# Kernel optimization log

Measured on AMD Instinct MI355X. Metric: run time of the kernel, lower is better.

## Reference

```python
import jax, jax.numpy as jnp
import numpy as np

# PGA G(3,0,1) blade layout: [1, e0,e1,e2,e3, e01,e02,e03,e12,e13,e23, e012,e013,e023,e123, e0123]
GRADE = jnp.array([0, 1, 1, 1, 1, 2, 2, 2, 2, 2, 2, 3, 3, 3, 3, 4])
# invariant inner product uses only blades not containing the degenerate e0
INNER_IDX = jnp.array([0, 2, 3, 4, 8, 9, 10, 14])

B, N, IN_MV, IN_S = 1, 1024, 16, 128
H, HID_MV, HID_S = 8, 4, 32
C_Z, OUT_MV, OUT_S = 128, 16, 128
ROPE_BASE = 4096.0


def equi_linear(mv, w5):
    # grade-wise equivariant channel mixing: w5 [out, in, 5] -> per-blade weight [out, in, 16]
    w16 = w5[:, :, GRADE]
    return jnp.einsum('...ib,oib->...ob', mv, w16)


def rope(x, base=ROPE_BASE):
    # rotary positional encoding along item axis 1; last dim must be even
    n, d = x.shape[1], x.shape[-1]
    half = d // 2
    freqs = base ** (-jnp.arange(half, dtype=x.dtype) / half)
    ang = jnp.arange(n, dtype=x.dtype)[:, None] * freqs  # [N, half]
    shp = (1, n) + (1,) * (x.ndim - 3) + (half,)
    cos, sin = jnp.cos(ang).reshape(shp), jnp.sin(ang).reshape(shp)
    x1, x2 = x[..., 0::2], x[..., 1::2]
    return jnp.stack([x1 * cos - x2 * sin, x1 * sin + x2 * cos], axis=-1).reshape(x.shape)


def setup_inputs() -> dict:
    key = jax.random.key(0)
    ks = jax.random.split(key, 16)
    sc_mv = 1.0 / np.sqrt(IN_MV)
    sc_s = 1.0 / np.sqrt(IN_S)
    return {
        'mv': jax.random.normal(ks[0], (B, N, IN_MV, 16), jnp.float32),
        's': jax.random.normal(ks[1], (B, N, IN_S), jnp.float32),
        'z': jax.random.normal(ks[2], (B, N, N, C_Z), jnp.float32),
        'q_w_mv': jax.random.normal(ks[3], (H * HID_MV, IN_MV, 5), jnp.float32) * sc_mv,
        'q_w_s': jax.random.normal(ks[4], (H * HID_S, IN_S), jnp.float32) * sc_s,
        'k_w_mv': jax.random.normal(ks[5], (HID_MV, IN_MV, 5), jnp.float32) * sc_mv,
        'k_w_s': jax.random.normal(ks[6], (HID_S, IN_S), jnp.float32) * sc_s,
        'v_w_mv': jax.random.normal(ks[7], (HID_MV, IN_MV, 5), jnp.float32) * sc_mv,
        'v_w_s': jax.random.normal(ks[8], (HID_S, IN_S), jnp.float32) * sc_s,
        'out_w_mv': jax.random.normal(ks[9], (OUT_MV, H * HID_MV, 5), jnp.float32) / np.sqrt(H * HID_MV),
        'out_w_s': jax.random.normal(ks[10], (OUT_S, H * HID_S), jnp.float32) / np.sqrt(H * HID_S),
        'ln_g': jnp.ones((C_Z,), jnp.float32),
        'ln_b': jnp.zeros((C_Z,), jnp.float32),
        'bias_w': jax.random.normal(ks[11], (C_Z, H), jnp.float32) / np.sqrt(C_Z),
    }


def reference(mv, s, z, q_w_mv, q_w_s, k_w_mv, k_w_s, v_w_mv, v_w_s,
              out_w_mv, out_w_s, ln_g, ln_b, bias_w):
    b, n = mv.shape[0], mv.shape[1]
    # multi-query QKV: queries per-head, shared single-head K/V
    q_mv = equi_linear(mv, q_w_mv).reshape(b, n, H, HID_MV, 16)
    q_s = jnp.einsum('bns,os->bno', s, q_w_s).reshape(b, n, H, HID_S)
    k_mv = equi_linear(mv, k_w_mv)                     # [B,N,hid_mv,16]
    k_s = jnp.einsum('bns,os->bno', s, k_w_s)          # [B,N,hid_s]
    v_mv = equi_linear(mv, v_w_mv)
    v_s = jnp.einsum('bns,os->bno', s, v_w_s)
    # rotary encoding on scalar queries/keys
    q_s, k_s = rope(q_s), rope(k_s)
    # invariant attention features: non-degenerate mv components + scalars
    qf = jnp.concatenate([q_mv[..., INNER_IDX].reshape(b, n, H, HID_MV * 8), q_s], axis=-1)
    kf = jnp.concatenate([k_mv[..., INNER_IDX].reshape(b, n, HID_MV * 8), k_s], axis=-1)
    d = qf.shape[-1]
    logits = jnp.einsum('bqhd,bkd->bhqk', qf, kf) / jnp.sqrt(jnp.asarray(d, qf.dtype))
    # pair bias: Linear(LayerNorm(z)) -> heads
    mu = jnp.mean(z, axis=-1, keepdims=True)
    var = jnp.var(z, axis=-1, keepdims=True)
    zn = (z - mu) * jax.lax.rsqrt(var + 1e-5) * ln_g + ln_b
    bias = jnp.einsum('bqkc,ch->bhqk', zn, bias_w)
    attn = jax.nn.softmax(logits + bias, axis=-1)      # [B,H,N,N]
    o_mv = jnp.einsum('bhqk,bkcx->bqhcx', attn, v_mv).reshape(b, n, H * HID_MV, 16)
    o_s = jnp.einsum('bhqk,bkc->bqhc', attn, v_s).reshape(b, n, H * HID_S)
    out_mv = equi_linear(o_mv, out_w_mv)               # [B,N,out_mv,16]
    out_s = jnp.einsum('bnc,oc->bno', o_s, out_w_s)    # [B,N,out_s]
    return out_mv, out_s
```

## Files before the change

### kernel.cpp

```cpp
#include <hip/hip_runtime.h>
#include <hip/hip_bf16.h>

__device__ __constant__ int GRADE_C[16] = {0,1,1,1,1,2,2,2,2,2,2,3,3,3,3,4};
__device__ __constant__ int INNER_C[8]  = {0,2,3,4,8,9,10,14};

#define OFF_GH    0
#define GWBT_BYTE 4096
#define KFB_BYTE  16384
#define VTB_BYTE  262144
#define QFB_BYTE  524288

typedef __attribute__((ext_vector_type(8))) short bf16x8;
typedef __attribute__((ext_vector_type(4))) float f32x4;
typedef __attribute__((ext_vector_type(4))) unsigned int u32x4;

static __device__ __forceinline__ unsigned short f2bf(float f) {
    unsigned int u = __float_as_uint(f);
    u = u + 0x7fffu + ((u >> 16) & 1u);
    return (unsigned short)(u >> 16);
}
static __device__ __forceinline__ unsigned pk2(float lo, float hi) {
    return (unsigned)f2bf(lo) | ((unsigned)f2bf(hi) << 16);
}
static __device__ __forceinline__ unsigned cvtpk(float lo, float hi) {
    __hip_bfloat162 c = __float22bfloat162_rn(make_float2(lo, hi));
    unsigned u;
    __builtin_memcpy(&u, &c, 4);
    return u;
}
static __device__ __forceinline__ float bflo(unsigned int u) {
    return __uint_as_float(u << 16);
}
static __device__ __forceinline__ float bfhi(unsigned int u) {
    return __uint_as_float(u & 0xffff0000u);
}

#define LDS_BAR() do { \
    asm volatile("s_waitcnt lgkmcnt(0)" ::: "memory"); \
    __builtin_amdgcn_s_barrier(); \
} while (0)

__global__ __launch_bounds__(256) void kproj(
    const float* __restrict__ mv, const float* __restrict__ s,
    const float* __restrict__ q_w_mv, const float* __restrict__ q_w_s,
    const float* __restrict__ k_w_mv, const float* __restrict__ k_w_s,
    const float* __restrict__ v_w_mv, const float* __restrict__ v_w_s,
    const float* __restrict__ ln_g, const float* __restrict__ ln_b,
    const float* __restrict__ bias_w, float* __restrict__ ws)
{
    __shared__ __align__(16) float mvn[256];
    __shared__ __align__(16) float sn[128];
    __shared__ float qs_pre[256];
    __shared__ float ks_pre[32];
    __shared__ float vs_pre[32];
    const int n = blockIdx.x, t = threadIdx.x;

    unsigned short* kfb = (unsigned short*)((char*)ws + KFB_BYTE);
    unsigned short* qfb = (unsigned short*)((char*)ws + QFB_BYTE);
    unsigned short* gwp = (unsigned short*)((char*)ws + GWBT_BYTE);
    unsigned short* vtb = (unsigned short*)((char*)ws + VTB_BYTE);

    mvn[t] = mv[n * 256 + t];
    if (t < 128) sn[t] = s[n * 128 + t];
    __syncthreads();

    {
        const float4* w = (const float4*)(q_w_s + t * 128);
        const float4* sv = (const float4*)sn;
        float acc = 0.f;
        #pragma unroll
        for (int c4 = 0; c4 < 32; ++c4) {
            float4 wv = w[c4], x = sv[c4];
            acc += wv.x * x.x + wv.y * x.y + wv.z * x.z + wv.w * x.w;
        }
        qs_pre[t] = acc;
    }
    if (t < 64) {
        const float* wb = (t < 32) ? (k_w_s + t * 128) : (v_w_s + (t - 32) * 128);
        const float4* w = (const float4*)wb;
        const float4* sv = (const float4*)sn;
        float acc = 0.f;
        #pragma unroll
        for (int c4 = 0; c4 < 32; ++c4) {
            float4 wv = w[c4], x = sv[c4];
            acc += wv.x * x.x + wv.y * x.y + wv.z * x.z + wv.w * x.w;
        }
        if (t < 32) ks_pre[t] = acc; else vs_pre[t - 32] = acc;
    }
    {
        int o = t >> 3, j = t & 7;
        int bx = INNER_C[j], g = GRADE_C[bx];
        float acc = 0.f;
        #pragma unroll
        for (int i = 0; i < 16; ++i)
            acc += mvn[i * 16 + bx] * q_w_mv[(o * 16 + i) * 5 + g];
        int h = o >> 2, c = o & 3, d = c * 8 + j;
        qfb[n * 1024 + h * 64 + d] = f2bf(acc);
    }
    {
        int hp = 8 + (t >> 5), d = t & 31;
        qfb[n * 1024 + hp * 64 + d] = 0;
        qfb[n * 1024 + hp * 64 + 32 + d] = 0;
    }
    if (t < 32) {
        int bx = INNER_C[t & 7], g = GRADE_C[bx];
        float acc = 0.f;
        #pragma unroll
        for (int i = 0; i < 16; ++i)
            acc += mvn[i * 16 + bx] * k_w_mv[((t >> 3) * 16 + i) * 5 + g];
        kfb[n * 64 + t] = f2bf(acc);
    }
    if (t >= 64 && t < 128) {
        int idx = t - 64, x = idx & 15, g = GRADE_C[x];
        float acc = 0.f;
        #pragma unroll
        for (int i = 0; i < 16; ++i)
            acc += mvn[i * 16 + x] * v_w_mv[((idx >> 4) * 16 + i) * 5 + g];
        vtb[idx * 1024 + n] = f2bf(acc);
    }
    __syncthreads();

    {
        int h = t >> 5, dd = t & 31, i = dd >> 1;
        float freq = exp2f(-0.75f * (float)i);
        float ang = (float)n * freq;
        float cv = cosf(ang), sv = sinf(ang);
        float x1 = qs_pre[h * 32 + 2 * i], x2 = qs_pre[h * 32 + 2 * i + 1];
        float val = ((dd & 1) == 0) ? (x1 * cv - x2 * sv) : (x1 * sv + x2 * cv);
        qfb[n * 1024 + h * 64 + 32 + dd] = f2bf(val);
    }
    if (t < 32) {
        int i = t >> 1;
        float freq = exp2f(-0.75f * (float)i);
        float ang = (float)n * freq;
        float cv = cosf(ang), sv = sinf(ang);
        float x1 = ks_pre[2 * i], x2 = ks_pre[2 * i + 1];
        float val = ((t & 1) == 0) ? (x1 * cv - x2 * sv) : (x1 * sv + x2 * cv);
        kfb[n * 64 + 32 + t] = f2bf(val);
    }
    if (t >= 32 && t < 64) vtb[(64 + t - 32) * 1024 + n] = f2bf(vs_pre[t - 32]);

    if (n == 0) {
        if (t < 128) {
            int cb = t >> 5, r = t & 31;
            int lg, e;
            if (r < 16) { lg = r >> 2; e = r & 3; }
            else        { lg = (r - 16) >> 2; e = 4 + (r & 3); }
            int pos = cb * 32 + lg * 8 + e;
            float g = ln_g[t];
            #pragma unroll
            for (int j = 0; j < 8; ++j)
                gwp[j * 128 + pos] = f2bf(g * bias_w[t * 8 + j]);
            gwp[8 * 128 + pos] = 0x3F80;
            #pragma unroll
            for (int j = 9; j < 16; ++j) gwp[j * 128 + pos] = 0;
        }
        if (t >= 128 && t < 136) {
            int h = t - 128;
            float gh = 0.f, ch = 0.f;
            for (int c = 0; c < 128; ++c) {
                gh += ln_g[c] * bias_w[c * 8 + h];
                ch += ln_b[c] * bias_w[c * 8 + h];
            }
            ws[OFF_GH + h] = gh;
            ws[OFF_GH + 8 + h] = ch;
        }
    }
}

__global__ __launch_bounds__(256, 3) void kfused(
    const float* __restrict__ z, const float* __restrict__ ws,
    const float* __restrict__ out_w_mv, const float* __restrict__ out_w_s,
    float* __restrict__ d_out)
{
    __shared__ float d1[128][17];
    __shared__ float d2[128][17];
    __shared__ float ssq[128];
    __shared__ float GhCh_s[16];
    __shared__ __align__(16) unsigned int Pb[8 * 512];
    __shared__ float inv_l[8];
    __shared__ float o_sh[8 * 96];

    const int q = blockIdx.x, t = threadIdx.x;
    const int w = t >> 6, l = t & 63, lm = l & 15, lg = l >> 4;

    if (t < 16) GhCh_s[t] = ws[OFF_GH + t];

    bf16x8 B1[4], B2[2];
    #pragma unroll
    for (int ks = 0; ks < 4; ++ks)
        B1[ks] = *(const bf16x8*)((const char*)ws + GWBT_BYTE + (lm * 128 + ks * 32 + lg * 8) * 2);
    #pragma unroll
    for (int ds = 0; ds < 2; ++ds)
        B2[ds] = *(const bf16x8*)((const char*)ws + QFB_BYTE + ((size_t)q * 1024 + lm * 64 + ds * 32 + lg * 8) * 2);

    const unsigned short* kfb = (const unsigned short*)((const char*)ws + KFB_BYTE);

    for (int kb = 0; kb < 8; ++kb) {
        float4 za[2][4], zb[2][4];
        bf16x8 A2[2][2];
        #pragma unroll
        for (int mi = 0; mi < 2; ++mi) {
            const int krow = kb * 128 + (w * 2 + mi) * 16 + lm;
            const float* zr = z + ((size_t)q * 1024 + krow) * 128 + lg * 4;
            #pragma unroll
            for (int ks = 0; ks < 4; ++ks) {
                za[mi][ks] = *(const float4*)(zr + ks * 32);
                zb[mi][ks] = *(const float4*)(zr + ks * 32 + 16);
            }
            #pragma unroll
            for (int ds = 0; ds < 2; ++ds)
                A2[mi][ds] = *(const bf16x8*)(kfb + (size_t)krow * 64 + ds * 32 + lg * 8);
        }

        if (kb > 0 && t < 128) {
            const int p = t >> 1, hg = t & 1;
            const int rr0 = 2 * p, rr1 = rr0 + 1;
            float mean0 = d1[rr0][8] * (1.f / 128.f);
            float var0  = ssq[rr0] * (1.f / 128.f) - mean0 * mean0;
            float rs0   = rsqrtf(var0 + 1e-5f);
            float mean1 = d1[rr1][8] * (1.f / 128.f);
            float var1  = ssq[rr1] * (1.f / 128.f) - mean1 * mean1;
            float rs1   = rsqrtf(var1 + 1e-5f);
            const int wbase = (kb - 1) * 64 + p;
            #pragma unroll
            for (int j = 0; j < 4; ++j) {
                int h = hg * 4 + j;
                float b0 = rs0 * (d1[rr0][h] - mean0 * GhCh_s[h]) + GhCh_s[8 + h];
                float s0 = d2[rr0][h] * 0.125f + b0;
                float b1 = rs1 * (d1[rr1][h] - mean1 * GhCh_s[h]) + GhCh_s[8 + h];
                float s1 = d2[rr1][h] * 0.125f + b1;
                Pb[h * 512 + (wbase ^ (h << 2))] = pk2(s0, s1);
            }
        }
        LDS_BAR();

        #pragma unroll
        for (int mi = 0; mi < 2; ++mi) {
            const int mt = w * 2 + mi;
            f32x4 acc1 = {0.f, 0.f, 0.f, 0.f};
            f32x4 acc2 = {0.f, 0.f, 0.f, 0.f};
            float sq = 0.f;
            #pragma unroll
            for (int ks = 0; ks < 4; ++ks) {
                float4 A = za[mi][ks], Bv = zb[mi][ks];
                sq = __builtin_fmaf(A.x, A.x, sq);   sq = __builtin_fmaf(A.y, A.y, sq);
                sq = __builtin_fmaf(A.z, A.z, sq);   sq = __builtin_fmaf(A.w, A.w, sq);
                sq = __builtin_fmaf(Bv.x, Bv.x, sq); sq = __builtin_fmaf(Bv.y, Bv.y, sq);
                sq = __builtin_fmaf(Bv.z, Bv.z, sq); sq = __builtin_fmaf(Bv.w, Bv.w, sq);
                u32x4 au;
                au[0] = cvtpk(A.x, A.y);   au[1] = cvtpk(A.z, A.w);
                au[2] = cvtpk(Bv.x, Bv.y); au[3] = cvtpk(Bv.z, Bv.w);
                bf16x8 af = __builtin_bit_cast(bf16x8, au);
                acc1 = __builtin_amdgcn_mfma_f32_16x16x32_bf16(af, B1[ks], acc1, 0, 0, 0);
            }
            acc2 = __builtin_amdgcn_mfma_f32_16x16x32_bf16(A2[mi][0], B2[0], acc2, 0, 0, 0);
            acc2 = __builtin_amdgcn_mfma_f32_16x16x32_bf16(A2[mi][1], B2[1], acc2, 0, 0, 0);

            sq += __shfl_xor(sq, 16);
            sq += __shfl_xor(sq, 32);
            if (lg == 0) ssq[mt * 16 + lm] = sq;

            #pragma unroll
            for (int r = 0; r < 4; ++r) {
                int row = mt * 16 + lg * 4 + r;
                d1[row][lm] = acc1[r];
                d2[row][lm] = acc2[r];
            }
        }
        LDS_BAR();
    }

    if (t < 128) {
        const int p = t >> 1, hg = t & 1;
        const int rr0 = 2 * p, rr1 = rr0 + 1;
        float mean0 = d1[rr0][8] * (1.f / 128.f);
        float var0  = ssq[rr0] * (1.f / 128.f) - mean0 * mean0;
        float rs0   = rsqrtf(var0 + 1e-5f);
        float mean1 = d1[rr1][8] * (1.f / 128.f);
        float var1  = ssq[rr1] * (1.f / 128.f) - mean1 * mean1;
        float rs1   = rsqrtf(var1 + 1e-5f);
        const int wbase = 7 * 64 + p;
        #pragma unroll
        for (int j = 0; j < 4; ++j) {
            int h = hg * 4 + j;
            float b0 = rs0 * (d1[rr0][h] - mean0 * GhCh_s[h]) + GhCh_s[8 + h];
            float s0 = d2[rr0][h] * 0.125f + b0;
            float b1 = rs1 * (d1[rr1][h] - mean1 * GhCh_s[h]) + GhCh_s[8 + h];
            float s1 = d2[rr1][h] * 0.125f + b1;
            Pb[h * 512 + (wbase ^ (h << 2))] = pk2(s0, s1);
        }
    }
    __syncthreads();

    {
        const int h = t >> 5, e = t & 31, hx = h << 2;
        unsigned int* Ph = &Pb[h * 512];
        float m = -1e30f;
        #pragma unroll
        for (int j = 0; j < 16; ++j) {
            unsigned int v = Ph[(e + j * 32) ^ hx];
            m = fmaxf(m, fmaxf(bflo(v), bfhi(v)));
        }
        #pragma unroll
        for (int d = 16; d >= 1; d >>= 1) m = fmaxf(m, __shfl_xor(m, d));
        float lsum = 0.f;
        #pragma unroll
        for (int j = 0; j < 16; ++j) {
            int idx = (e + j * 32) ^ hx;
            unsigned int v = Ph[idx];
            float p0 = __expf(bflo(v) - m);
            float p1 = __expf(bfhi(v) - m);
            lsum += p0 + p1;
            Ph[idx] = pk2(p0, p1);
        }
        #pragma unroll
        for (int d = 16; d >= 1; d >>= 1) lsum += __shfl_xor(lsum, d);
        if (e == 0) inv_l[h] = 1.f / lsum;
    }
    __syncthreads();

    {
        const unsigned short* vtb = (const unsigned short*)((const char*)ws + VTB_BYTE);
        const char* PbB = (const char*)Pb;
        const int hh = lm & 7;
        const int nmt = (w < 2) ? 2 : 1;
        for (int ii = 0; ii < nmt; ++ii) {
            int mt = w + ii * 4;
            f32x4 acc = {0.f, 0.f, 0.f, 0.f};
            #pragma unroll 8
            for (int ks = 0; ks < 32; ++ks) {
                bf16x8 a = *(const bf16x8*)(vtb + (size_t)(mt * 16 + lm) * 1024 + ks * 32 + lg * 8);
                bf16x8 b = *(const bf16x8*)(PbB + hh * 2048 + ((ks * 64 + lg * 16) ^ (hh << 4)));
                acc = __builtin_amdgcn_mfma_f32_16x16x32_bf16(a, b, acc, 0, 0, 0);
            }
            if (lm < 8) {
                float il = inv_l[lm];
                #pragma unroll
                for (int r = 0; r < 4; ++r)
                    o_sh[lm * 96 + mt * 16 + lg * 4 + r] = acc[r] * il;
            }
        }
    }
    __syncthreads();

    {
        int o2 = t >> 4, b = t & 15, g = GRADE_C[b];
        float acc = 0.f;
        #pragma unroll
        for (int i = 0; i < 32; ++i)
            acc += o_sh[(i >> 2) * 96 + (i & 3) * 16 + b] *
                   out_w_mv[(o2 * 32 + i) * 5 + g];
        d_out[(q * 16 + o2) * 16 + b] = acc;
    }
    if (t < 128) {
        const float* wv2 = out_w_s + t * 256;
        float acc = 0.f;
        #pragma unroll 4
        for (int c = 0; c < 256; ++c)
            acc += o_sh[(c >> 5) * 96 + 64 + (c & 31)] * wv2[c];
        d_out[262144 + q * 128 + t] = acc;
    }
}

extern "C" void kernel_launch(void* const* d_in, const int* in_sizes, int n_in,
                              void* d_out, int out_size, void* d_ws, size_t ws_size,
                              hipStream_t stream) {
    (void)in_sizes; (void)n_in; (void)out_size; (void)ws_size;
    const float* mv       = (const float*)d_in[0];
    const float* s        = (const float*)d_in[1];
    const float* z        = (const float*)d_in[2];
    const float* q_w_mv   = (const float*)d_in[3];
    const float* q_w_s    = (const float*)d_in[4];
    const float* k_w_mv   = (const float*)d_in[5];
    const float* k_w_s    = (const float*)d_in[6];
    const float* v_w_mv   = (const float*)d_in[7];
    const float* v_w_s    = (const float*)d_in[8];
    const float* out_w_mv = (const float*)d_in[9];
    const float* out_w_s  = (const float*)d_in[10];
    const float* ln_g     = (const float*)d_in[11];
    const float* ln_b     = (const float*)d_in[12];
    const float* bias_w   = (const float*)d_in[13];
    float* ws  = (float*)d_ws;
    float* out = (float*)d_out;

    kproj<<<1024, 256, 0, stream>>>(mv, s, q_w_mv, q_w_s, k_w_mv, k_w_s,
                                    v_w_mv, v_w_s, ln_g, ln_b, bias_w, ws);
    kfused<<<1024, 256, 0, stream>>>(z, ws, out_w_mv, out_w_s, out);
}
```

Baseline: 178.1 us.

## Register double-buffer z loads and finalize pair bias in-wave with shuffles

Replaces the 8-iteration loop, which staged MFMA results through LDS (d1/d2/ssq) with two block barriers per iteration, with 16 phases of 64 rows each. Each wave computes LayerNorm statistics and the bias/logit combination directly from its MFMA accumulators using lane shuffles, then writes packed bf16 scores to Pb. The next phase's z tile is prefetched into a second register buffer while the current one is processed. This removes the per-iteration barriers and LDS round trips so that loading z overlaps with compute, at the cost of more vector registers, which may lower occupancy under launch_bounds(256,3).

```diff
diff --git a/kernel.cpp b/kernel.cpp
--- a/kernel.cpp
+++ b/kernel.cpp
@@ -34,11 +34,6 @@
 static __device__ __forceinline__ float bfhi(unsigned int u) {
     return __uint_as_float(u & 0xffff0000u);
 }
-
-#define LDS_BAR() do { \
-    asm volatile("s_waitcnt lgkmcnt(0)" ::: "memory"); \
-    __builtin_amdgcn_s_barrier(); \
-} while (0)
 
 __global__ __launch_bounds__(256) void kproj(
     const float* __restrict__ mv, const float* __restrict__ s,
@@ -173,18 +168,12 @@
     const float* __restrict__ out_w_mv, const float* __restrict__ out_w_s,
     float* __restrict__ d_out)
 {
-    __shared__ float d1[128][17];
-    __shared__ float d2[128][17];
-    __shared__ float ssq[128];
-    __shared__ float GhCh_s[16];
     __shared__ __align__(16) unsigned int Pb[8 * 512];
     __shared__ float inv_l[8];
     __shared__ float o_sh[8 * 96];
 
     const int q = blockIdx.x, t = threadIdx.x;
     const int w = t >> 6, l = t & 63, lm = l & 15, lg = l >> 4;
-
-    if (t < 16) GhCh_s[t] = ws[OFF_GH + t];
 
     bf16x8 B1[4], B2[2];
     #pragma unroll
@@ -195,101 +184,69 @@
         B2[ds] = *(const bf16x8*)((const char*)ws + QFB_BYTE + ((size_t)q * 1024 + lm * 64 + ds * 32 + lg * 8) * 2);
 
     const unsigned short* kfb = (const unsigned short*)((const char*)ws + KFB_BYTE);
-
-    for (int kb = 0; kb < 8; ++kb) {
-        float4 za[2][4], zb[2][4];
-        bf16x8 A2[2][2];
-        #pragma unroll
-        for (int mi = 0; mi < 2; ++mi) {
-            const int krow = kb * 128 + (w * 2 + mi) * 16 + lm;
-            const float* zr = z + ((size_t)q * 1024 + krow) * 128 + lg * 4;
-            #pragma unroll
-            for (int ks = 0; ks < 4; ++ks) {
-                za[mi][ks] = *(const float4*)(zr + ks * 32);
-                zb[mi][ks] = *(const float4*)(zr + ks * 32 + 16);
-            }
-            #pragma unroll
-            for (int ds = 0; ds < 2; ++ds)
-                A2[mi][ds] = *(const bf16x8*)(kfb + (size_t)krow * 64 + ds * 32 + lg * 8);
-        }
-
-        if (kb > 0 && t < 128) {
-            const int p = t >> 1, hg = t & 1;
-            const int rr0 = 2 * p, rr1 = rr0 + 1;
-            float mean0 = d1[rr0][8] * (1.f / 128.f);
-            float var0  = ssq[rr0] * (1.f / 128.f) - mean0 * mean0;
-            float rs0   = rsqrtf(var0 + 1e-5f);
-            float mean1 = d1[rr1][8] * (1.f / 128.f);
-            float var1  = ssq[rr1] * (1.f / 128.f) - mean1 * mean1;
-            float rs1   = rsqrtf(var1 + 1e-5f);
-            const int wbase = (kb - 1) * 64 + p;
-            #pragma unroll
-            for (int j = 0; j < 4; ++j) {
-                int h = hg * 4 + j;
-                float b0 = rs0 * (d1[rr0][h] - mean0 * GhCh_s[h]) + GhCh_s[8 + h];
-                float s0 = d2[rr0][h] * 0.125f + b0;
-                float b1 = rs1 * (d1[rr1][h] - mean1 * GhCh_s[h]) + GhCh_s[8 + h];
-                float s1 = d2[rr1][h] * 0.125f + b1;
-                Pb[h * 512 + (wbase ^ (h << 2))] = pk2(s0, s1);
-            }
-        }
-        LDS_BAR();
-
-        #pragma unroll
-        for (int mi = 0; mi < 2; ++mi) {
-            const int mt = w * 2 + mi;
-            f32x4 acc1 = {0.f, 0.f, 0.f, 0.f};
-            f32x4 acc2 = {0.f, 0.f, 0.f, 0.f};
-            float sq = 0.f;
-            #pragma unroll
-            for (int ks = 0; ks < 4; ++ks) {
-                float4 A = za[mi][ks], Bv = zb[mi][ks];
-                sq = __builtin_fmaf(A.x, A.x, sq);   sq = __builtin_fmaf(A.y, A.y, sq);
-                sq = __builtin_fmaf(A.z, A.z, sq);   sq = __builtin_fmaf(A.w, A.w, sq);
-                sq = __builtin_fmaf(Bv.x, Bv.x, sq); sq = __builtin_fmaf(Bv.y, Bv.y, sq);
-                sq = __builtin_fmaf(Bv.z, Bv.z, sq); sq = __builtin_fmaf(Bv.w, Bv.w, sq);
-                u32x4 au;
-                au[0] = cvtpk(A.x, A.y);   au[1] = cvtpk(A.z, A.w);
-                au[2] = cvtpk(Bv.x, Bv.y); au[3] = cvtpk(Bv.z, Bv.w);
-                bf16x8 af = __builtin_bit_cast(bf16x8, au);
-                acc1 = __builtin_amdgcn_mfma_f32_16x16x32_bf16(af, B1[ks], acc1, 0, 0, 0);
-            }
-            acc2 = __builtin_amdgcn_mfma_f32_16x16x32_bf16(A2[mi][0], B2[0], acc2, 0, 0, 0);
-            acc2 = __builtin_amdgcn_mfma_f32_16x16x32_bf16(A2[mi][1], B2[1], acc2, 0, 0, 0);
-
-            sq += __shfl_xor(sq, 16);
-            sq += __shfl_xor(sq, 32);
-            if (lg == 0) ssq[mt * 16 + lm] = sq;
-
-            #pragma unroll
-            for (int r = 0; r < 4; ++r) {
-                int row = mt * 16 + lg * 4 + r;
-                d1[row][lm] = acc1[r];
-                d2[row][lm] = acc2[r];
-            }
-        }
-        LDS_BAR();
-    }
-
-    if (t < 128) {
-        const int p = t >> 1, hg = t & 1;
-        const int rr0 = 2 * p, rr1 = rr0 + 1;
-        float mean0 = d1[rr0][8] * (1.f / 128.f);
-        float var0  = ssq[rr0] * (1.f / 128.f) - mean0 * mean0;
-        float rs0   = rsqrtf(var0 + 1e-5f);
-        float mean1 = d1[rr1][8] * (1.f / 128.f);
-        float var1  = ssq[rr1] * (1.f / 128.f) - mean1 * mean1;
-        float rs1   = rsqrtf(var1 + 1e-5f);
-        const int wbase = 7 * 64 + p;
-        #pragma unroll
-        for (int j = 0; j < 4; ++j) {
-            int h = hg * 4 + j;
-            float b0 = rs0 * (d1[rr0][h] - mean0 * GhCh_s[h]) + GhCh_s[8 + h];
-            float s0 = d2[rr0][h] * 0.125f + b0;
-            float b1 = rs1 * (d1[rr1][h] - mean1 * GhCh_s[h]) + GhCh_s[8 + h];
-            float s1 = d2[rr1][h] * 0.125f + b1;
-            Pb[h * 512 + (wbase ^ (h << 2))] = pk2(s0, s1);
-        }
+    const float Gh_l = ws[OFF_GH + (lm & 7)];
+    const float Ch_l = ws[OFF_GH + 8 + (lm & 7)];
+    const char* zq = (const char*)z + (size_t)q * 1024 * 512;
+
+    float4 zA[8], zB[8];
+
+#define LOADZ(p, Z) do {                                                        \
+    const char* zr_ = zq + (size_t)((p) * 64 + w * 16 + lm) * 512 + lg * 16;    \
+    Z[0] = *(const float4*)(zr_);        Z[4] = *(const float4*)(zr_ + 64);     \
+    Z[1] = *(const float4*)(zr_ + 128);  Z[5] = *(const float4*)(zr_ + 192);    \
+    Z[2] = *(const float4*)(zr_ + 256);  Z[6] = *(const float4*)(zr_ + 320);    \
+    Z[3] = *(const float4*)(zr_ + 384);  Z[7] = *(const float4*)(zr_ + 448);    \
+} while (0)
+
+#define PHASE(p, ZC, ZN) do {                                                   \
+    const int krow_ = (p) * 64 + w * 16 + lm;                                   \
+        \
+    bf16x8 A2a_ = *(const bf16x8*)(kfb + (size_t)krow_ * 64 + lg * 8);          \
+    bf16x8 A2b_ = *(const bf16x8*)(kfb + (size_t)krow_ * 64 + 32 + lg * 8);     \
+    if ((p) < 15) LOADZ((p) + 1, ZN);                                           \
+    f32x4 acc1 = {0.f, 0.f, 0.f, 0.f};                                          \
+    f32x4 acc2 = {0.f, 0.f, 0.f, 0.f};                                          \
+    float sq = 0.f;                                                             \
+    _Pragma("unroll")                                                           \
+    for (int ks = 0; ks < 4; ++ks) {                                            \
+        float4 A = ZC[ks], Bv = ZC[4 + ks];                                     \
+        sq = __builtin_fmaf(A.x, A.x, sq);   sq = __builtin_fmaf(A.y, A.y, sq); \
+        sq = __builtin_fmaf(A.z, A.z, sq);   sq = __builtin_fmaf(A.w, A.w, sq); \
+        sq = __builtin_fmaf(Bv.x, Bv.x, sq); sq = __builtin_fmaf(Bv.y, Bv.y, sq);\
+        sq = __builtin_fmaf(Bv.z, Bv.z, sq); sq = __builtin_fmaf(Bv.w, Bv.w, sq);\
+        u32x4 au;                                                               \
+        au[0] = cvtpk(A.x, A.y);   au[1] = cvtpk(A.z, A.w);                     \
+        au[2] = cvtpk(Bv.x, Bv.y); au[3] = cvtpk(Bv.z, Bv.w);                   \
+        bf16x8 af = __builtin_bit_cast(bf16x8, au);                             \
+        acc1 = __builtin_amdgcn_mfma_f32_16x16x32_bf16(af, B1[ks], acc1, 0, 0, 0);\
+    }                                                                           \
+    acc2 = __builtin_amdgcn_mfma_f32_16x16x32_bf16(A2a_, B2[0], acc2, 0, 0, 0); \
+    acc2 = __builtin_amdgcn_mfma_f32_16x16x32_bf16(A2b_, B2[1], acc2, 0, 0, 0); \
+    sq += __shfl_xor(sq, 16);                                                   \
+    sq += __shfl_xor(sq, 32);                                                   \
+    float sval[4];                                                              \
+    _Pragma("unroll")                                                           \
+    for (int r = 0; r < 4; ++r) {                                               \
+        float ssq_r = __shfl(sq, lg * 4 + r);                                   \
+        float sum_r = __shfl(acc1[r], lg * 16 + 8);                             \
+        float mean = sum_r * (1.f / 128.f);                                     \
+        float var  = ssq_r * (1.f / 128.f) - mean * mean;                       \
+        float rs   = rsqrtf(var + 1e-5f);                                       \
+        float bias = rs * (acc1[r] - mean * Gh_l) + Ch_l;                       \
+        sval[r] = acc2[r] * 0.125f + bias;                                      \
+    }                                                                           \
+    if (lm < 8) {                                                               \
+        int wp = (p) * 32 + w * 8 + lg * 2;                                     \
+        Pb[lm * 512 + ( wp      ^ (lm << 2))] = cvtpk(sval[0], sval[1]);        \
+        Pb[lm * 512 + ((wp + 1) ^ (lm << 2))] = cvtpk(sval[2], sval[3]);        \
+    }                                                                           \
+} while (0)
+
+    LOADZ(0, zA);
+    #pragma unroll
+    for (int pp = 0; pp < 8; ++pp) {
+        PHASE(2 * pp,     zA, zB);
+        PHASE(2 * pp + 1, zB, zA);
     }
     __syncthreads();
 
@@ -361,6 +318,8 @@
             acc += o_sh[(c >> 5) * 96 + 64 + (c & 31)] * wv2[c];
         d_out[262144 + q * 128 + t] = acc;
     }
+#undef PHASE
+#undef LOADZ
 }
 
 extern "C" void kernel_launch(void* const* d_in, const int* in_sizes, int n_in,
```

New measurement: 174.4 us. 1.02x faster.
